# Performance work log

Measured on AMD Instinct MI355X. Metric: run time of the kernel, lower is better.

Reference implementation:

```python
import jax, jax.numpy as jnp
import numpy as np

B, N, K, H, C, PE, EMB, OUT = 2, 2048, 16, 4, 8, 64, 1024, 2
P = C * (C + 1) // 2  # 36 unordered class pairs
RADIUS, NEG, EPS = 0.08, 0.2, 1e-5


def _ball_query(pos, radius, nsample):
    # pos [B,N,2] -> idx [B,N,nsample]; indices within radius, padded with first in-ball index
    sq = jnp.sum(pos * pos, -1)
    d = sq[:, :, None] + sq[:, None, :] - 2.0 * jnp.einsum('bnc,bmc->bnm', pos, pos)
    n = pos.shape[1]
    idx = jnp.broadcast_to(jnp.arange(n)[None, None, :], d.shape)
    idx = jnp.where(d > radius * radius, n, idx)
    idx = jnp.sort(idx, axis=-1)[:, :, :nsample]
    return jnp.where(idx == n, idx[:, :, :1], idx)


def _gather(feat, idx):
    # feat [B,F,N], idx [B,N,K] -> [B,F,N,K]
    return jnp.take_along_axis(feat[:, :, None, :], idx[:, None, :, :], axis=3)


def _pe(rel, dim):
    # sinusoidal encoding of relative coords rel [B,2,N,K] -> [B,dim,N,K]
    nf = dim // 4
    freqs = 10000.0 ** (-jnp.arange(nf, dtype=rel.dtype) / nf)
    ang = rel[:, :, None] * freqs[None, None, :, None, None]     # [B,2,nf,N,K]
    enc = jnp.concatenate([jnp.sin(ang), jnp.cos(ang)], axis=2)  # [B,2,2nf,N,K]
    b = enc.shape[0]
    return enc.reshape(b, dim, enc.shape[3], enc.shape[4])


def _conv(x, w, g, bvec):
    # 1x1 conv (no bias) + inference BN (running mean 0, var 1) + LeakyReLU
    y = jnp.einsum('oc,bc...->bo...', w, x) / jnp.sqrt(1.0 + EPS)
    sh = (1, -1) + (1,) * (y.ndim - 2)
    return jax.nn.leaky_relu(y * g.reshape(sh) + bvec.reshape(sh), NEG)


def _attn_layer(x, Ws, a_pairs, a_selfs, core, tgt):
    # PointpairAttentionLayer (per-class-pair coefficients), vmapped over heads.
    # x [B,F,N,K]; core [B,N] int; tgt [B,N,K] int
    s0 = jnp.minimum(tgt, core[:, :, None])
    s1 = jnp.maximum(tgt, core[:, :, None])
    pidx = s0 * C - (s0 * (s0 - 1)) // 2 + (s1 - s0)             # [B,N,K] pair index
    self_mask = (tgt[:, :, 0] < core)[:, :, None]                # slot-0 keeps a_self when pair-write happened earlier

    def head(W, a_pair, a_self):
        Wh = jnp.einsum('bfnk,fg->bnkg', x, W)                   # [B,N,K,F]
        a = a_pair[pidx]                                         # [B,N,K,F]
        slot0 = jnp.where(self_mask, a_self[core], a[:, :, 0])
        a = a.at[:, :, 0].set(slot0)
        e = jax.nn.leaky_relu(Wh * a, NEG)
        attn = jax.nn.softmax(e, axis=2)                         # over K neighbors
        return jax.nn.elu(attn * Wh)                             # [B,N,K,F]

    hs = jax.vmap(head)(Ws, a_pairs, a_selfs)                    # [H,B,N,K,F]
    b, n, k = x.shape[0], x.shape[2], x.shape[3]
    return jnp.transpose(hs, (1, 0, 4, 2, 3)).reshape(b, -1, n, k)


def _edge(feat, idx):
    # DGCNN edge features: concat(neighbor - center, center)
    tf = _gather(feat, idx)
    return jnp.concatenate([tf - feat[..., None],
                            jnp.broadcast_to(feat[..., None], tf.shape)], axis=1)


def _forward(pos, types, conv1_w, bn1_g, bn1_b, W1, ap1, as1,
             conv2_w, bn2_g, bn2_b, W2, ap2, as2,
             conv3_w, bn3_g, bn3_b, W3, ap3, as3,
             conv4_w, bn4_g, bn4_b, W4, ap4, as4,
             conv5_w, bn5_g, bn5_b, lin1_w, bn6_g, bn6_b,
             lin2_w, lin2_b, bn7_g, bn7_b, lin3_w, lin3_b):
    idx = _ball_query(pos, RADIUS, K)                            # [B,N,K]
    posT = jnp.transpose(pos, (0, 2, 1))                         # [B,2,N]
    rel = _gather(posT, idx) - posT[..., None]                   # [B,2,N,K]
    tgt = _gather(types[:, None, :], idx)[:, 0]                  # [B,N,K] neighbor classes

    x = _conv(_pe(rel, PE), conv1_w, bn1_g, bn1_b)               # [B,64,N,K]
    x1 = _attn_layer(x, W1, ap1, as1, types, tgt).sum(-1)        # [B,H*64,N]
    x = _conv(_edge(x1, idx), conv2_w, bn2_g, bn2_b)             # [B,64,N,K]
    x2 = _attn_layer(x, W2, ap2, as2, types, tgt).sum(-1)        # [B,H*64,N]
    x = _conv(_edge(x2, idx), conv3_w, bn3_g, bn3_b)             # [B,128,N,K]
    x3 = _attn_layer(x, W3, ap3, as3, types, tgt).sum(-1)        # [B,H*128,N]
    x = _conv(_edge(x3, idx), conv4_w, bn4_g, bn4_b)             # [B,256,N,K]
    x4 = _attn_layer(x, W4, ap4, as4, types, tgt).sum(-1)        # [B,H*256,N]

    xc = jnp.concatenate([x1, x2, x3, x4], axis=1)               # [B,H*512,N]
    x = _conv(xc, conv5_w, bn5_g, bn5_b)                         # [B,EMB,N]
    feat = jnp.concatenate([x.max(-1), x.mean(-1)], axis=-1)     # [B,2*EMB]

    def bn1d(y, g, bvec):
        return (y / jnp.sqrt(1.0 + EPS)) * g + bvec

    h = jax.nn.leaky_relu(bn1d(feat @ lin1_w.T, bn6_g, bn6_b), NEG)
    h = jax.nn.leaky_relu(bn1d(h @ lin2_w.T + lin2_b, bn7_g, bn7_b), NEG)
    return h @ lin3_w.T + lin3_b                                 # [B,OUT]


def setup_inputs() -> dict:
    key = jax.random.key(0)
    ks = iter(jax.random.split(key, 64))
    rn = lambda *s: jax.random.normal(next(ks), s, dtype=jnp.float32)
    d = {}
    d['pos'] = jax.random.uniform(next(ks), (B, N, 2), dtype=jnp.float32)
    d['types'] = jax.random.randint(next(ks), (B, N), 0, C, dtype=jnp.int32)

    def layer(f_in, f, tag):
        d['conv%d_w' % tag] = rn(f, f_in) * (1.0 / np.sqrt(f_in))
        d['bn%d_g' % tag] = jnp.ones((f,), jnp.float32)
        d['bn%d_b' % tag] = jnp.zeros((f,), jnp.float32)

    layer(PE, 64, 1)
    d['W1'] = rn(H, 64, 64) * 0.125; d['ap1'] = rn(H, P, 64) * 0.5; d['as1'] = rn(H, C, 64) * 0.5
    layer(2 * H * 64, 64, 2)
    d['W2'] = rn(H, 64, 64) * 0.125; d['ap2'] = rn(H, P, 64) * 0.5; d['as2'] = rn(H, C, 64) * 0.5
    layer(2 * H * 64, 128, 3)
    d['W3'] = rn(H, 128, 128) * 0.09; d['ap3'] = rn(H, P, 128) * 0.5; d['as3'] = rn(H, C, 128) * 0.5
    layer(2 * H * 128, 256, 4)
    d['W4'] = rn(H, 256, 256) * 0.0625; d['ap4'] = rn(H, P, 256) * 0.5; d['as4'] = rn(H, C, 256) * 0.5
    layer(H * 512, EMB, 5)
    d['lin1_w'] = rn(512, 2 * EMB) * 0.02
    d['bn6_g'] = jnp.ones((512,), jnp.float32); d['bn6_b'] = jnp.zeros((512,), jnp.float32)
    d['lin2_w'] = rn(256, 512) * 0.04; d['lin2_b'] = jnp.zeros((256,), jnp.float32)
    d['bn7_g'] = jnp.ones((256,), jnp.float32); d['bn7_b'] = jnp.zeros((256,), jnp.float32)
    d['lin3_w'] = rn(OUT, 256) * 0.06; d['lin3_b'] = jnp.zeros((OUT,), jnp.float32)
    return d


def reference(pos, types, conv1_w, bn1_g, bn1_b, W1, ap1, as1,
              conv2_w, bn2_g, bn2_b, W2, ap2, as2,
              conv3_w, bn3_g, bn3_b, W3, ap3, as3,
              conv4_w, bn4_g, bn4_b, W4, ap4, as4,
              conv5_w, bn5_g, bn5_b, lin1_w, bn6_g, bn6_b,
              lin2_w, lin2_b, bn7_g, bn7_b, lin3_w, lin3_b):
    return _forward(pos, types, conv1_w, bn1_g, bn1_b, W1, ap1, as1,
                    conv2_w, bn2_g, bn2_b, W2, ap2, as2,
                    conv3_w, bn3_g, bn3_b, W3, ap3, as3,
                    conv4_w, bn4_g, bn4_b, W4, ap4, as4,
                    conv5_w, bn5_g, bn5_b, lin1_w, bn6_g, bn6_b,
                    lin2_w, lin2_b, bn7_g, bn7_b, lin3_w, lin3_b)
```

## Files before the change

### kernel.cpp

```cpp
#include <hip/hip_runtime.h>
#include <math.h>

#define BB 2
#define NN 2048
#define KK 16
#define HH 4
#define CC 8
#define PP 36
#define NEGS 0.2f
#define INVS 0.9999950000374997f

typedef __attribute__((ext_vector_type(8))) short s16x8;
typedef __attribute__((ext_vector_type(8))) unsigned short u16x8;
typedef __attribute__((ext_vector_type(4))) float f32x4;

__device__ inline unsigned short bfh(float x) {
  unsigned u = __float_as_uint(x);
  return (unsigned short)((u + 0x7FFFu + ((u >> 16) & 1u)) >> 16);
}
__device__ inline float bff(unsigned short h) {
  return __uint_as_float(((unsigned)h) << 16);
}
__device__ inline f32x4 mfma16(s16x8 a, s16x8 b, f32x4 c) {
  return __builtin_amdgcn_mfma_f32_16x16x32_bf16(a, b, c, 0, 0, 0);
}

__global__ __launch_bounds__(256) void k_ballquery(const float* __restrict__ pos,
                                                   const int* __restrict__ types,
                                                   int* __restrict__ idxg,
                                                   int* __restrict__ acode,
                                                   float* __restrict__ rel) {
  __shared__ int s_buf[4][KK];
  const float r2 = (float)(0.08 * 0.08);
  int wslot = threadIdx.x >> 6;
  int lane = threadIdx.x & 63;
  int wg = blockIdx.x * 4 + wslot;
  int b = wg / NN, n = wg - b * NN;
  const float* pb = pos + (size_t)b * NN * 2;
  float px = pb[n * 2 + 0], py = pb[n * 2 + 1];
  float sqn = px * px + py * py;
  unsigned mask = 0u;
  int base = lane * 32;
  for (int j = 0; j < 32; ++j) {
    float qx = pb[(base + j) * 2 + 0], qy = pb[(base + j) * 2 + 1];
    float sqm = qx * qx + qy * qy;
    float d = sqn + sqm - 2.0f * (px * qx + py * qy);
    if (d <= r2) mask |= (1u << j);
  }
  int cnt = __popc(mask);
  int inc = cnt;
#pragma unroll
  for (int off = 1; off < 64; off <<= 1) {
    int v = __shfl_up(inc, off, 64);
    if (lane >= off) inc += v;
  }
  int total = __shfl(inc, 63, 64);
  int excl = inc - cnt;
  unsigned mm = mask;
  int p = excl;
  while (mm && p < KK) {
    int j = __ffs(mm) - 1;
    mm &= mm - 1u;
    s_buf[wslot][p] = base + j;
    ++p;
  }
  __syncthreads();
  int tc = total < KK ? total : KK;
  if (lane < KK) {
    int m0 = s_buf[wslot][0];
    int mk = (lane < tc) ? s_buf[wslot][lane] : m0;
    idxg[wg * KK + lane] = mk;
    int core = types[b * NN + n];
    int tg = types[b * NN + mk];
    int s0 = tg < core ? tg : core;
    int s1 = tg < core ? core : tg;
    int code = s0 * CC - (s0 * (s0 - 1)) / 2 + (s1 - s0);
    if (lane == 0 && tg < core) code = PP + core;
    acode[wg * KK + lane] = code;
    rel[(wg * KK + lane) * 2 + 0] = pb[mk * 2 + 0] - px;
    rel[(wg * KK + lane) * 2 + 1] = pb[mk * 2 + 1] - py;
  }
}

struct PackDesc {
  const float* src;
  unsigned short* dh;
  unsigned short* dl;
  int KB, NT, srcld, Cdiff, mode, sstride, dstride, nrep, bpr;
};
struct PackArgs {
  PackDesc d[12];
};
__global__ __launch_bounds__(256) void k_megapack(PackArgs pa) {
  PackDesc D = pa.d[blockIdx.y];
  int rep = blockIdx.x / D.bpr;
  if (rep >= D.nrep) return;
  int f = (blockIdx.x - rep * D.bpr) * 256 + threadIdx.x;
  int total = D.KB * D.NT * 64;
  if (f >= total) return;
  const float* src = D.src + (size_t)rep * D.sstride;
  unsigned short* dh = D.dh + (size_t)rep * D.dstride;
  unsigned short* dl = D.dl + (size_t)rep * D.dstride;
  int l = f & 63;
  int t2 = f >> 6;
  int n = (t2 / D.KB) * 16 + (l & 15);
  int k0 = (t2 % D.KB) * 32 + ((l >> 4) * 8);
  size_t o = (size_t)t2 * 512 + (size_t)l * 8;
#pragma unroll
  for (int i = 0; i < 8; ++i) {
    int k = k0 + i;
    float v;
    if (D.mode == 0) {
      v = src[(size_t)k * D.srcld + n];
    } else if (D.mode == 1) {
      v = src[(size_t)n * D.srcld + k];
    } else {
      v = src[(size_t)n * D.srcld + k + D.Cdiff] - src[(size_t)n * D.srcld + k];
    }
    unsigned short hi = bfh(v);
    dh[o + i] = hi;
    dl[o + i] = bfh(v - bff(hi));
  }
}

template <int KBW, int NTB>
__global__ __launch_bounds__(512, 4) void k_pregemm(
    const unsigned short* __restrict__ xh, const unsigned short* __restrict__ xl,
    int xoff, const unsigned short* __restrict__ wph,
    const unsigned short* __restrict__ wpl, const float* __restrict__ scale,
    const float* __restrict__ bias, unsigned short* __restrict__ ouh,
    unsigned short* __restrict__ oul, int cout) {
  constexpr int NCH = KBW / 2;
  constexpr int JT = NTB / 2;
  const int KBT = KBW;
  const int ld = 2 * cout;
  __shared__ alignas(16) char s_mem[65536];
  int tid = threadIdx.x;
  int lane = tid & 63;
  int w = tid >> 6;
  int lg = lane >> 4;
  int ln = lane & 15;
  int bm = blockIdx.x;
  int ntoff = blockIdx.y * NTB;
  int wm = w >> 1, wn = w & 1;
  f32x4 acc[2][JT];
#pragma unroll
  for (int m = 0; m < 2; ++m)
#pragma unroll
    for (int j = 0; j < JT; ++j) acc[m][j] = (f32x4){0.f, 0.f, 0.f, 0.f};

  int srowg = bm * 128 + w * 16 + ln;
  const unsigned short* gH = xh + (size_t)srowg * 2048 + xoff + lg * 8;
  const unsigned short* gL = xl + (size_t)srowg * 2048 + xoff + lg * 8;
  int wbyA = ((w * 2 + 0) * 64 + lane) * 16;
  int wbyB = ((w * 2 + 1) * 64 + lane) * 16;
  u16x8 h0, h1, l0, l1;
  auto load4 = [&](int ch) {
    h0 = *(const u16x8*)(gH + ch * 64);
    h1 = *(const u16x8*)(gH + ch * 64 + 32);
    l0 = *(const u16x8*)(gL + ch * 64);
    l1 = *(const u16x8*)(gL + ch * 64 + 32);
  };
  load4(0);
  *(u16x8*)(s_mem + wbyA) = h0;
  *(u16x8*)(s_mem + wbyB) = h1;
  *(u16x8*)(s_mem + wbyA + 16384) = l0;
  *(u16x8*)(s_mem + wbyB + 16384) = l1;
  __syncthreads();
  int p = 0;
  for (int ch = 0; ch < NCH; ++ch) {
    if (ch + 1 < NCH) load4(ch + 1);
#pragma unroll
    for (int ks = 0; ks < 2; ++ks) {
      s16x8 ah[2], al[2];
#pragma unroll
      for (int m = 0; m < 2; ++m) {
        int by = p * 32768 + (((wm * 2 + m) * 2 + ks) * 64 + lane) * 16;
        ah[m] = *(const s16x8*)(s_mem + by);
        al[m] = *(const s16x8*)(s_mem + by + 16384);
      }
      int kb = ch * 2 + ks;
      __builtin_amdgcn_s_setprio(1);
#pragma unroll
      for (int j = 0; j < JT; ++j) {
        size_t fo = ((size_t)(ntoff + wn * JT + j) * KBT + kb) * 64 + lane;
        s16x8 bh = ((const s16x8*)wph)[fo];
        s16x8 bl = ((const s16x8*)wpl)[fo];
#pragma unroll
        for (int m = 0; m < 2; ++m) {
          acc[m][j] = mfma16(ah[m], bh, acc[m][j]);
          acc[m][j] = mfma16(al[m], bh, acc[m][j]);
          acc[m][j] = mfma16(ah[m], bl, acc[m][j]);
        }
      }
      __builtin_amdgcn_s_setprio(0);
    }
    if (ch + 1 < NCH) {
      int d = (p ^ 1) * 32768;
      *(u16x8*)(s_mem + d + wbyA) = h0;
      *(u16x8*)(s_mem + d + wbyB) = h1;
      *(u16x8*)(s_mem + d + wbyA + 16384) = l0;
      *(u16x8*)(s_mem + d + wbyB + 16384) = l1;
      p ^= 1;
    }
    __syncthreads();
  }
#pragma unroll
  for (int j = 0; j < JT; ++j) {
    int g = (ntoff + wn * JT + j) * 16 + ln;
    int gm = g >= cout ? g - cout : g;
    float sc = scale[gm] * INVS;
    float bs = (g >= cout) ? bias[gm] : 0.f;
#pragma unroll
    for (int m = 0; m < 2; ++m) {
#pragma unroll
      for (int reg = 0; reg < 4; ++reg) {
        int row = bm * 128 + wm * 32 + m * 16 + lg * 4 + reg;
        float v = acc[m][j][reg] * sc + bs;
        unsigned short hi = bfh(v);
        ouh[(size_t)row * ld + g] = hi;
        oul[(size_t)row * ld + g] = bfh(v - bff(hi));
      }
    }
  }
}

template <int FOUT>
__global__ __launch_bounds__(512, 4) void k_attn(
    unsigned short* xh, unsigned short* xl,
    const unsigned short* __restrict__ uvh, const unsigned short* __restrict__ uvl,
    const int* __restrict__ idx, const int* __restrict__ acode,
    const unsigned short* __restrict__ attnh, const unsigned short* __restrict__ attnl,
    const float* __restrict__ ap, const float* __restrict__ as_, int ooff) {
  constexpr int KBA = FOUT / 32;
  constexpr int NT = FOUT / 16;
  constexpr int NTW_A = NT / 2;
  constexpr int JW = (NTW_A > 2) ? 2 : NTW_A;
  constexpr int NPASS = NTW_A / JW;
  constexpr int YPLANE = 64 * FOUT * 2;
  constexpr int FPW = (4 * KBA) / 8;
  constexpr int C2 = 2 * FOUT;

  __shared__ alignas(16) char s_mem[2 * YPLANE];
  __shared__ int s_gsrc[64];
  __shared__ int s_code[64];

  int tid = threadIdx.x;
  int lane = tid & 63;
  int w = tid >> 6;
  int lg = lane >> 4;
  int ln = lane & 15;
  int pgbase = blockIdx.x * 4;

  if (tid < 64) {
    int pg = pgbase + (tid >> 4);
    int b = pg >> 11;
    s_gsrc[tid] = b * 2048 + idx[pg * KK + (tid & 15)];
    s_code[tid] = acode[pg * KK + (tid & 15)];
  }
  __syncthreads();

#pragma unroll
  for (int r = 0; r < FPW; ++r) {
    int f = w * FPW + r;
    int mt = f / KBA, kb = f % KBA;
    int row = mt * 16 + ln;
    int col = kb * 32 + lg * 8;
    int gsrc = s_gsrc[row];
    int ctr = pgbase + mt;
    u16x8 a = *(const u16x8*)(uvh + (size_t)gsrc * C2 + col);
    u16x8 b_ = *(const u16x8*)(uvl + (size_t)gsrc * C2 + col);
    u16x8 c_ = *(const u16x8*)(uvh + (size_t)ctr * C2 + FOUT + col);
    u16x8 d_ = *(const u16x8*)(uvl + (size_t)ctr * C2 + FOUT + col);
    unsigned short oh[8], olo[8];
#pragma unroll
    for (int i = 0; i < 8; ++i) {
      float vv = (bff(a[i]) + bff(b_[i])) + (bff(c_[i]) + bff(d_[i]));
      vv = (vv >= 0.f) ? vv : NEGS * vv;
      unsigned short hi = bfh(vv);
      oh[i] = hi;
      olo[i] = bfh(vv - bff(hi));
    }
    *(u16x8*)(s_mem + (f * 64 + lane) * 16) = *(u16x8*)oh;
    *(u16x8*)(s_mem + YPLANE + (f * 64 + lane) * 16) = *(u16x8*)olo;
  }
  __syncthreads();

  {
    int h = w >> 1, nh = w & 1;
    const s16x8* wph = (const s16x8*)(attnh + (size_t)h * FOUT * FOUT);
    const s16x8* wpl = (const s16x8*)(attnl + (size_t)h * FOUT * FOUT);
    const float* aph = ap + (size_t)h * PP * FOUT;
    const float* ash = as_ + (size_t)h * CC * FOUT;
    for (int pass = 0; pass < NPASS; ++pass) {
      f32x4 aacc[4][JW];
#pragma unroll
      for (int m = 0; m < 4; ++m)
#pragma unroll
        for (int j = 0; j < JW; ++j) aacc[m][j] = (f32x4){0.f, 0.f, 0.f, 0.f};
#pragma unroll 2
      for (int kb = 0; kb < KBA; ++kb) {
        s16x8 ah[4], al[4];
#pragma unroll
        for (int m = 0; m < 4; ++m) {
          int by = ((m * KBA + kb) * 64 + lane) * 16;
          ah[m] = *(const s16x8*)(s_mem + by);
          al[m] = *(const s16x8*)(s_mem + YPLANE + by);
        }
        __builtin_amdgcn_s_setprio(1);
#pragma unroll
        for (int j = 0; j < JW; ++j) {
          int nt = nh * NTW_A + pass * JW + j;
          size_t fo = ((size_t)nt * KBA + kb) * 64 + lane;
          s16x8 bh = wph[fo];
          s16x8 bl = wpl[fo];
#pragma unroll
          for (int m = 0; m < 4; ++m) {
            aacc[m][j] = mfma16(ah[m], bh, aacc[m][j]);
            aacc[m][j] = mfma16(al[m], bh, aacc[m][j]);
            aacc[m][j] = mfma16(ah[m], bl, aacc[m][j]);
          }
        }
        __builtin_amdgcn_s_setprio(0);
      }
#pragma unroll
      for (int m = 0; m < 4; ++m) {
        int pg = pgbase + m;
#pragma unroll
        for (int j = 0; j < JW; ++j) {
          int nt = nh * NTW_A + pass * JW + j;
          int g = nt * 16 + ln;
          float wv[4], e[4];
          float mx = -3.0e38f;
#pragma unroll
          for (int reg = 0; reg < 4; ++reg) {
            int code = s_code[m * 16 + lg * 4 + reg];
            const float* tb = (code < PP) ? (aph + (size_t)code * FOUT)
                                          : (ash + (size_t)(code - PP) * FOUT);
            float a = tb[g];
            float t = aacc[m][j][reg];
            wv[reg] = t;
            float ev = t * a;
            ev = (ev >= 0.f) ? ev : NEGS * ev;
            e[reg] = ev;
            mx = fmaxf(mx, ev);
          }
          mx = fmaxf(mx, __shfl_xor(mx, 16, 64));
          mx = fmaxf(mx, __shfl_xor(mx, 32, 64));
          float ssum = 0.f;
#pragma unroll
          for (int reg = 0; reg < 4; ++reg) {
            float pe = __expf(e[reg] - mx);
            e[reg] = pe;
            ssum += pe;
          }
          ssum += __shfl_xor(ssum, 16, 64);
          ssum += __shfl_xor(ssum, 32, 64);
          float inv = 1.f / ssum;
          float o = 0.f;
#pragma unroll
          for (int reg = 0; reg < 4; ++reg) {
            float u = e[reg] * inv * wv[reg];
            o += (u > 0.f) ? u : (__expf(u) - 1.f);
          }
          o += __shfl_xor(o, 16, 64);
          o += __shfl_xor(o, 32, 64);
          if (lane < 16) {
            size_t oc = (size_t)pg * 2048 + ooff + h * FOUT + g;
            unsigned short hi = bfh(o);
            xh[oc] = hi;
            xl[oc] = bfh(o - bff(hi));
          }
        }
      }
    }
  }
}

template <int CPREV, int FOUT, bool L1M>
__global__ __launch_bounds__(512, 4) void k_layer_m(
    unsigned short* xh, unsigned short* xl, int xoff,
    const float* __restrict__ rel, const int* __restrict__ idx,
    const int* __restrict__ acode,
    const unsigned short* __restrict__ convh, const unsigned short* __restrict__ convl,
    const unsigned short* __restrict__ attnh, const unsigned short* __restrict__ attnl,
    const float* __restrict__ bng, const float* __restrict__ bnb,
    const float* __restrict__ ap, const float* __restrict__ as_, int ooff) {
  constexpr int K_TOT = L1M ? CPREV : 2 * CPREV;
  constexpr int KB = K_TOT / 32;
  constexpr int NT = FOUT / 16;
  constexpr int NT_W = NT / 4;
  constexpr int NTW_A = NT / 2;
  constexpr int JW = (NTW_A > 2) ? 2 : NTW_A;
  constexpr int NPASS = NTW_A / JW;
  constexpr int KBA = FOUT / 32;
  constexpr int YPLANE = 64 * FOUT * 2;
  constexpr int S_BYTES = (2 * YPLANE > 32768) ? 2 * YPLANE : 32768;

  __shared__ alignas(16) char s_mem[S_BYTES];
  __shared__ int s_gsrc[64];
  __shared__ int s_code[64];

  int tid = threadIdx.x;
  int lane = tid & 63;
  int w = tid >> 6;
  int lg = lane >> 4;
  int ln = lane & 15;
  int pgbase = blockIdx.x * 4;

  if (tid < 64) {
    int pg = pgbase + (tid >> 4);
    int b = pg >> 11;
    s_gsrc[tid] = b * 2048 + idx[pg * KK + (tid & 15)];
    s_code[tid] = acode[pg * KK + (tid & 15)];
  }
  __syncthreads();

  int smt = w >> 1, skb = w & 1;
  int wby0 = (w * 64 + lane) * 16;

  int wr = w >> 2, wc = w & 3;
  f32x4 cacc[2][NT_W];
#pragma unroll
  for (int m = 0; m < 2; ++m)
#pragma unroll
    for (int j = 0; j < NT_W; ++j) cacc[m][j] = (f32x4){0.f, 0.f, 0.f, 0.f};

  auto compute_chunk = [&](int ch, int p) {
#pragma unroll
    for (int ks = 0; ks < 2; ++ks) {
      s16x8 ah[2], al[2];
#pragma unroll
      for (int m = 0; m < 2; ++m) {
        int by = p * 16384 + (((wr * 2 + m) * 2 + ks) * 64 + lane) * 16;
        ah[m] = *(const s16x8*)(s_mem + by);
        al[m] = *(const s16x8*)(s_mem + by + 8192);
      }
      int kb = ch * 2 + ks;
      __builtin_amdgcn_s_setprio(1);
#pragma unroll
      for (int j = 0; j < NT_W; ++j) {
        size_t fo = ((size_t)(wc * NT_W + j) * KB + kb) * 64 + lane;
        s16x8 bh = ((const s16x8*)convh)[fo];
        s16x8 bl = ((const s16x8*)convl)[fo];
#pragma unroll
        for (int m = 0; m < 2; ++m) {
          cacc[m][j] = mfma16(ah[m], bh, cacc[m][j]);
          cacc[m][j] = mfma16(al[m], bh, cacc[m][j]);
          cacc[m][j] = mfma16(ah[m], bl, cacc[m][j]);
        }
      }
      __builtin_amdgcn_s_setprio(0);
    }
  };

  if constexpr (L1M) {
    float rc = rel[((size_t)(pgbase + smt) * KK + ln) * 2 + skb];
    unsigned short hb[8], lb[8];
#pragma unroll
    for (int i = 0; i < 8; ++i) {
      int j = lg * 8 + i;
      int fidx = j & 15;
      float freq = exp2f(-(float)fidx * 0.8304820237218406f);
      float ang = rc * freq;
      float v = (j < 16) ? __sinf(ang) : __cosf(ang);
      unsigned short hi = bfh(v);
      hb[i] = hi;
      lb[i] = bfh(v - bff(hi));
    }
    *(u16x8*)(s_mem + wby0) = *(u16x8*)hb;
    *(u16x8*)(s_mem + wby0 + 8192) = *(u16x8*)lb;
    __syncthreads();
    compute_chunk(0, 0);
    __syncthreads();
  }

#pragma unroll
  for (int j = 0; j < NT_W; ++j) {
    int g = (wc * NT_W + j) * 16 + ln;
    float sc = bng[g] * INVS;
    float bs = bnb[g];
    int gpart = ((g >> 5) * 64 + ((g >> 3) & 3) * 16) * 16 + (g & 7) * 2;
#pragma unroll
    for (int m = 0; m < 2; ++m) {
#pragma unroll
      for (int reg = 0; reg < 4; ++reg) {
        int r = wr * 32 + m * 16 + lg * 4 + reg;
        float v = cacc[m][j][reg] * sc + bs;
        v = (v >= 0.f) ? v : NEGS * v;
        unsigned short hi = bfh(v);
        unsigned short lo = bfh(v - bff(hi));
        int by = (r >> 4) * (KBA * 1024) + gpart + (r & 15) * 16;
        *(unsigned short*)(s_mem + by) = hi;
        *(unsigned short*)(s_mem + YPLANE + by) = lo;
      }
    }
  }
  __syncthreads();

  {
    int h = w >> 1, nh = w & 1;
    const s16x8* wph = (const s16x8*)(attnh + (size_t)h * FOUT * FOUT);
    const s16x8* wpl = (const s16x8*)(attnl + (size_t)h * FOUT * FOUT);
    const float* aph = ap + (size_t)h * PP * FOUT;
    const float* ash = as_ + (size_t)h * CC * FOUT;
    for (int pass = 0; pass < NPASS; ++pass) {
      f32x4 aacc[4][JW];
#pragma unroll
      for (int m = 0; m < 4; ++m)
#pragma unroll
        for (int j = 0; j < JW; ++j) aacc[m][j] = (f32x4){0.f, 0.f, 0.f, 0.f};
#pragma unroll 2
      for (int kb = 0; kb < KBA; ++kb) {
        s16x8 ah[4], al[4];
#pragma unroll
        for (int m = 0; m < 4; ++m) {
          int by = ((m * KBA + kb) * 64 + lane) * 16;
          ah[m] = *(const s16x8*)(s_mem + by);
          al[m] = *(const s16x8*)(s_mem + YPLANE + by);
        }
        __builtin_amdgcn_s_setprio(1);
#pragma unroll
        for (int j = 0; j < JW; ++j) {
          int nt = nh * NTW_A + pass * JW + j;
          size_t fo = ((size_t)nt * KBA + kb) * 64 + lane;
          s16x8 bh = wph[fo];
          s16x8 bl = wpl[fo];
#pragma unroll
          for (int m = 0; m < 4; ++m) {
            aacc[m][j] = mfma16(ah[m], bh, aacc[m][j]);
            aacc[m][j] = mfma16(al[m], bh, aacc[m][j]);
            aacc[m][j] = mfma16(ah[m], bl, aacc[m][j]);
          }
        }
        __builtin_amdgcn_s_setprio(0);
      }
#pragma unroll
      for (int m = 0; m < 4; ++m) {
        int pg = pgbase + m;
#pragma unroll
        for (int j = 0; j < JW; ++j) {
          int nt = nh * NTW_A + pass * JW + j;
          int g = nt * 16 + ln;
          float wv[4], e[4];
          float mx = -3.0e38f;
#pragma unroll
          for (int reg = 0; reg < 4; ++reg) {
            int code = s_code[m * 16 + lg * 4 + reg];
            const float* tb = (code < PP) ? (aph + (size_t)code * FOUT)
                                          : (ash + (size_t)(code - PP) * FOUT);
            float a = tb[g];
            float t = aacc[m][j][reg];
            wv[reg] = t;
            float ev = t * a;
            ev = (ev >= 0.f) ? ev : NEGS * ev;
            e[reg] = ev;
            mx = fmaxf(mx, ev);
          }
          mx = fmaxf(mx, __shfl_xor(mx, 16, 64));
          mx = fmaxf(mx, __shfl_xor(mx, 32, 64));
          float ssum = 0.f;
#pragma unroll
          for (int reg = 0; reg < 4; ++reg) {
            float pe = __expf(e[reg] - mx);
            e[reg] = pe;
            ssum += pe;
          }
          ssum += __shfl_xor(ssum, 16, 64);
          ssum += __shfl_xor(ssum, 32, 64);
          float inv = 1.f / ssum;
          float o = 0.f;
#pragma unroll
          for (int reg = 0; reg < 4; ++reg) {
            float u = e[reg] * inv * wv[reg];
            o += (u > 0.f) ? u : (__expf(u) - 1.f);
          }
          o += __shfl_xor(o, 16, 64);
          o += __shfl_xor(o, 32, 64);
          if (lane < 16) {
            size_t oc = (size_t)pg * 2048 + ooff + h * FOUT + g;
            unsigned short hi = bfh(o);
            xh[oc] = hi;
            xl[oc] = bfh(o - bff(hi));
          }
        }
      }
    }
  }
}

__global__ __launch_bounds__(512, 4) void k_gemm5_m(const unsigned short* __restrict__ xh,
                                                    const unsigned short* __restrict__ xl,
                                                    const unsigned short* __restrict__ bph,
                                                    const unsigned short* __restrict__ bpl,
                                                    const float* __restrict__ g5,
                                                    const float* __restrict__ b5,
                                                    float* __restrict__ pmax,
                                                    float* __restrict__ psum) {
  __shared__ alignas(16) char s_mem[65536];
  int tid = threadIdx.x;
  int lane = tid & 63;
  int w = tid >> 6;
  int lg = lane >> 4;
  int ln = lane & 15;
  int bm = blockIdx.x, bn = blockIdx.y;
  int wm = w >> 2, wn = w & 3;
  f32x4 acc[4][2];
#pragma unroll
  for (int m = 0; m < 4; ++m)
#pragma unroll
    for (int j = 0; j < 2; ++j) acc[m][j] = (f32x4){0.f, 0.f, 0.f, 0.f};

  int srowg = bm * 128 + w * 16 + ln;
  const unsigned short* gH = xh + (size_t)srowg * 2048 + lg * 8;
  const unsigned short* gL = xl + (size_t)srowg * 2048 + lg * 8;
  int wbyA = ((w * 2 + 0) * 64 + lane) * 16;
  int wbyB = ((w * 2 + 1) * 64 + lane) * 16;
  u16x8 h0, h1, l0, l1;
  auto load4 = [&](int ch) {
    h0 = *(const u16x8*)(gH + ch * 64);
    h1 = *(const u16x8*)(gH + ch * 64 + 32);
    l0 = *(const u16x8*)(gL + ch * 64);
    l1 = *(const u16x8*)(gL + ch * 64 + 32);
  };
  load4(0);
  *(u16x8*)(s_mem + wbyA) = h0;
  *(u16x8*)(s_mem + wbyB) = h1;
  *(u16x8*)(s_mem + wbyA + 16384) = l0;
  *(u16x8*)(s_mem + wbyB + 16384) = l1;
  __syncthreads();
  int p = 0;
  for (int ch = 0; ch < 32; ++ch) {
    if (ch + 1 < 32) load4(ch + 1);
#pragma unroll
    for (int ks = 0; ks < 2; ++ks) {
      s16x8 ah[4], al[4];
#pragma unroll
      for (int m = 0; m < 4; ++m) {
        int by = p * 32768 + (((wm * 4 + m) * 2 + ks) * 64 + lane) * 16;
        ah[m] = *(const s16x8*)(s_mem + by);
        al[m] = *(const s16x8*)(s_mem + by + 16384);
      }
      int kb = ch * 2 + ks;
      __builtin_amdgcn_s_setprio(1);
#pragma unroll
      for (int j = 0; j < 2; ++j) {
        size_t fo = ((size_t)(bn * 8 + wn * 2 + j) * 64 + kb) * 64 + lane;
        s16x8 bh = ((const s16x8*)bph)[fo];
        s16x8 bl = ((const s16x8*)bpl)[fo];
#pragma unroll
        for (int m = 0; m < 4; ++m) {
          acc[m][j] = mfma16(ah[m], bh, acc[m][j]);
          acc[m][j] = mfma16(al[m], bh, acc[m][j]);
          acc[m][j] = mfma16(ah[m], bl, acc[m][j]);
        }
      }
      __builtin_amdgcn_s_setprio(0);
    }
    if (ch + 1 < 32) {
      int d = (p ^ 1) * 32768;
      *(u16x8*)(s_mem + d + wbyA) = h0;
      *(u16x8*)(s_mem + d + wbyB) = h1;
      *(u16x8*)(s_mem + d + wbyA + 16384) = l0;
      *(u16x8*)(s_mem + d + wbyB + 16384) = l1;
      p ^= 1;
    }
    __syncthreads();
  }

  float cmax[2], csum[2];
#pragma unroll
  for (int j = 0; j < 2; ++j) {
    int g = bn * 128 + wn * 32 + j * 16 + ln;
    float sc = g5[g] * INVS;
    float bs = b5[g];
    float mx = -3.0e38f, sm = 0.f;
#pragma unroll
    for (int m = 0; m < 4; ++m)
#pragma unroll
      for (int reg = 0; reg < 4; ++reg) {
        float v = acc[m][j][reg] * sc + bs;
        v = (v >= 0.f) ? v : NEGS * v;
        mx = fmaxf(mx, v);
        sm += v;
      }
    mx = fmaxf(mx, __shfl_xor(mx, 16, 64));
    mx = fmaxf(mx, __shfl_xor(mx, 32, 64));
    sm += __shfl_xor(sm, 16, 64);
    sm += __shfl_xor(sm, 32, 64);
    cmax[j] = mx;
    csum[j] = sm;
  }
  float* s_f = (float*)s_mem;
  if (lg == 0) {
#pragma unroll
    for (int j = 0; j < 2; ++j) {
      int col = wn * 32 + j * 16 + ln;
      s_f[(wm * 128 + col) * 2 + 0] = cmax[j];
      s_f[(wm * 128 + col) * 2 + 1] = csum[j];
    }
  }
  __syncthreads();
  if (tid < 128) {
    float mx = fmaxf(s_f[tid * 2], s_f[(128 + tid) * 2]);
    float sm = s_f[tid * 2 + 1] + s_f[(128 + tid) * 2 + 1];
    pmax[(size_t)bm * 1024 + bn * 128 + tid] = mx;
    psum[(size_t)bm * 1024 + bn * 128 + tid] = sm;
  }
}

__global__ __launch_bounds__(256) void k_feat(const float* __restrict__ pmax,
                                              const float* __restrict__ psum,
                                              float* __restrict__ feat) {
  int t = blockIdx.x * 256 + threadIdx.x;
  if (t >= BB * 1024) return;
  int b = t >> 10, o = t & 1023;
  float mx = -3.0e38f, sm = 0.f;
  for (int i = 0; i < 16; ++i) {
    mx = fmaxf(mx, pmax[(size_t)(b * 16 + i) * 1024 + o]);
    sm += psum[(size_t)(b * 16 + i) * 1024 + o];
  }
  feat[b * 2048 + o] = mx;
  feat[b * 2048 + 1024 + o] = sm * (1.0f / NN);
}

template <bool HASB, bool DOBN, bool ACT>
__global__ __launch_bounds__(256) void k_head(const float* __restrict__ X,
                                              const float* __restrict__ Wm,
                                              const float* __restrict__ bias,
                                              const float* __restrict__ g,
                                              const float* __restrict__ bb,
                                              float* __restrict__ Y, int IN, int ON) {
  int gt = blockIdx.x * 256 + threadIdx.x;
  int w = gt >> 6, lane = gt & 63;
  if (w >= BB * ON) return;
  int b = w / ON, o = w - b * ON;
  const float* x = X + (size_t)b * IN;
  const float* wr = Wm + (size_t)o * IN;
  float s = 0.f;
  for (int c = lane; c < IN; c += 64) s += x[c] * wr[c];
#pragma unroll
  for (int off = 32; off > 0; off >>= 1) s += __shfl_down(s, off, 64);
  if (lane == 0) {
    if (HASB) s += bias[o];
    if (DOBN) s = s * INVS * g[o] + bb[o];
    if (ACT) s = (s >= 0.f) ? s : NEGS * s;
    Y[(size_t)b * ON + o] = s;
  }
}

extern "C" void kernel_launch(void* const* d_in, const int* in_sizes, int n_in,
                              void* d_out, int out_size, void* d_ws, size_t ws_size,
                              hipStream_t stream) {
  const float* pos = (const float*)d_in[0];
  const int* types = (const int*)d_in[1];
  const float* conv1_w = (const float*)d_in[2];
  const float* bn1_g = (const float*)d_in[3];
  const float* bn1_b = (const float*)d_in[4];
  const float* W1 = (const float*)d_in[5];
  const float* ap1 = (const float*)d_in[6];
  const float* as1 = (const float*)d_in[7];
  const float* conv2_w = (const float*)d_in[8];
  const float* bn2_g = (const float*)d_in[9];
  const float* bn2_b = (const float*)d_in[10];
  const float* W2 = (const float*)d_in[11];
  const float* ap2 = (const float*)d_in[12];
  const float* as2 = (const float*)d_in[13];
  const float* conv3_w = (const float*)d_in[14];
  const float* bn3_g = (const float*)d_in[15];
  const float* bn3_b = (const float*)d_in[16];
  const float* W3 = (const float*)d_in[17];
  const float* ap3 = (const float*)d_in[18];
  const float* as3 = (const float*)d_in[19];
  const float* conv4_w = (const float*)d_in[20];
  const float* bn4_g = (const float*)d_in[21];
  const float* bn4_b = (const float*)d_in[22];
  const float* W4 = (const float*)d_in[23];
  const float* ap4 = (const float*)d_in[24];
  const float* as4 = (const float*)d_in[25];
  const float* conv5_w = (const float*)d_in[26];
  const float* bn5_g = (const float*)d_in[27];
  const float* bn5_b = (const float*)d_in[28];
  const float* lin1_w = (const float*)d_in[29];
  const float* bn6_g = (const float*)d_in[30];
  const float* bn6_b = (const float*)d_in[31];
  const float* lin2_w = (const float*)d_in[32];
  const float* lin2_b = (const float*)d_in[33];
  const float* bn7_g = (const float*)d_in[34];
  const float* bn7_b = (const float*)d_in[35];
  const float* lin3_w = (const float*)d_in[36];
  const float* lin3_b = (const float*)d_in[37];
  (void)in_sizes; (void)n_in; (void)out_size; (void)ws_size;

  float* ws = (float*)d_ws;
  size_t off = 0;
  auto take = [&](size_t nf) {
    float* p = ws + off;
    off += (nf + 63) & ~(size_t)63;
    return p;
  };
  auto takeu = [&](size_t nu) { return (unsigned short*)take((nu + 1) / 2); };

  int* idx = (int*)take(BB * NN * KK);
  int* acode = (int*)take(BB * NN * KK);
  float* rel = take((size_t)BB * NN * KK * 2);
  unsigned short* xh = takeu((size_t)BB * NN * 2048);
  unsigned short* xl = takeu((size_t)BB * NN * 2048);
  unsigned short* uvh = takeu((size_t)4096 * 512);
  unsigned short* uvl = takeu((size_t)4096 * 512);
  float* pmax = take(32 * 1024);
  float* psum = take(32 * 1024);
  float* feat = take(BB * 2048);
  float* h1 = take(BB * 512);
  float* h2 = take(BB * 256);
  unsigned short* c1h = takeu(64 * 64);
  unsigned short* c1l = takeu(64 * 64);
  unsigned short* uvw2h = takeu(256 * 128);
  unsigned short* uvw2l = takeu(256 * 128);
  unsigned short* uvw3h = takeu(256 * 256);
  unsigned short* uvw3l = takeu(256 * 256);
  unsigned short* uvw4h = takeu(512 * 512);
  unsigned short* uvw4l = takeu(512 * 512);
  unsigned short* a1h = takeu(4 * 64 * 64);
  unsigned short* a1l = takeu(4 * 64 * 64);
  unsigned short* a2h = takeu(4 * 64 * 64);
  unsigned short* a2l = takeu(4 * 64 * 64);
  unsigned short* a3h = takeu(4 * 128 * 128);
  unsigned short* a3l = takeu(4 * 128 * 128);
  unsigned short* a4h = takeu(4 * 256 * 256);
  unsigned short* a4l = takeu(4 * 256 * 256);
  unsigned short* g5h = takeu((size_t)2048 * 1024);
  unsigned short* g5l = takeu((size_t)2048 * 1024);

  dim3 blk(256);
  dim3 blk5(512);

  PackArgs pa;
  pa.d[0] = {conv1_w, c1h, c1l, 2, 4, 64, 0, 1, 0, 0, 1, 2};
  pa.d[1] = {conv2_w, uvw2h, uvw2l, 8, 4, 512, 0, 1, 0, 0, 1, 8};
  pa.d[2] = {conv2_w, uvw2h + 16384, uvw2l + 16384, 8, 4, 512, 256, 2, 0, 0, 1, 8};
  pa.d[3] = {conv3_w, uvw3h, uvw3l, 8, 8, 512, 0, 1, 0, 0, 1, 16};
  pa.d[4] = {conv3_w, uvw3h + 32768, uvw3l + 32768, 8, 8, 512, 256, 2, 0, 0, 1, 16};
  pa.d[5] = {conv4_w, uvw4h, uvw4l, 16, 16, 1024, 0, 1, 0, 0, 1, 64};
  pa.d[6] = {conv4_w, uvw4h + 131072, uvw4l + 131072, 16, 16, 1024, 512, 2, 0, 0, 1, 64};
  pa.d[7] = {W1, a1h, a1l, 2, 4, 64, 0, 0, 4096, 4096, 4, 2};
  pa.d[8] = {W2, a2h, a2l, 2, 4, 64, 0, 0, 4096, 4096, 4, 2};
  pa.d[9] = {W3, a3h, a3l, 4, 8, 128, 0, 0, 16384, 16384, 4, 8};
  pa.d[10] = {W4, a4h, a4l, 8, 16, 256, 0, 0, 65536, 65536, 4, 32};
  pa.d[11] = {conv5_w, g5h, g5l, 64, 64, 2048, 0, 1, 0, 0, 1, 1024};
  k_megapack<<<dim3(1024, 12), blk, 0, stream>>>(pa);

  k_ballquery<<<dim3(BB * NN / 4), blk, 0, stream>>>(pos, types, idx, acode, rel);

  k_layer_m<64, 64, true><<<dim3(BB * NN / 4), blk5, 0, stream>>>(
      xh, xl, 0, rel, idx, acode, c1h, c1l, a1h, a1l, bn1_g, bn1_b, ap1, as1, 0);

  k_pregemm<8, 4><<<dim3(32, 2), blk5, 0, stream>>>(
      xh, xl, 0, uvw2h, uvw2l, bn2_g, bn2_b, uvh, uvl, 64);
  k_attn<64><<<dim3(BB * NN / 4), blk5, 0, stream>>>(
      xh, xl, uvh, uvl, idx, acode, a2h, a2l, ap2, as2, 256);

  k_pregemm<8, 8><<<dim3(32, 2), blk5, 0, stream>>>(
      xh, xl, 256, uvw3h, uvw3l, bn3_g, bn3_b, uvh, uvl, 128);
  k_attn<128><<<dim3(BB * NN / 4), blk5, 0, stream>>>(
      xh, xl, uvh, uvl, idx, acode, a3h, a3l, ap3, as3, 512);

  k_pregemm<16, 8><<<dim3(32, 4), blk5, 0, stream>>>(
      xh, xl, 512, uvw4h, uvw4l, bn4_g, bn4_b, uvh, uvl, 256);
  k_attn<256><<<dim3(BB * NN / 4), blk5, 0, stream>>>(
      xh, xl, uvh, uvl, idx, acode, a4h, a4l, ap4, as4, 1024);

  k_gemm5_m<<<dim3(32, 8), blk5, 0, stream>>>(xh, xl, g5h, g5l, bn5_g, bn5_b, pmax, psum);
  k_feat<<<dim3(8), blk, 0, stream>>>(pmax, psum, feat);
  k_head<false, true, true><<<dim3(BB * 512 * 64 / 256), blk, 0, stream>>>(
      feat, lin1_w, nullptr, bn6_g, bn6_b, h1, 2048, 512);
  k_head<true, true, true><<<dim3(BB * 256 * 64 / 256), blk, 0, stream>>>(
      h1, lin2_w, lin2_b, bn7_g, bn7_b, h2, 512, 256);
  k_head<true, false, false><<<dim3(1), blk, 0, stream>>>(
      h2, lin3_w, lin3_b, nullptr, nullptr, (float*)d_out, 256, 2);
}
```

Measured before the change: 429.2 us.

## Drop low-half activation splitting, store pre-GEMM in fp32, fuse head kernels

Activations are now kept only as a single bf16 plane instead of a hi/lo pair, which removes one of the three MFMAs per product and halves LDS staging and global traffic. The pre-GEMM output is written as fp32 rather than as two bf16 planes. The softmax max-subtraction is dropped. The feature reduction and three head layers are merged into one tail kernel. Precision of the activations falls to plain bf16, and removing the max subtraction risks exp overflow for large logits.

```diff
diff --git a/kernel.cpp b/kernel.cpp
--- a/kernel.cpp
+++ b/kernel.cpp
@@ -125,16 +125,14 @@
 
 template <int KBW, int NTB>
 __global__ __launch_bounds__(512, 4) void k_pregemm(
-    const unsigned short* __restrict__ xh, const unsigned short* __restrict__ xl,
-    int xoff, const unsigned short* __restrict__ wph,
-    const unsigned short* __restrict__ wpl, const float* __restrict__ scale,
-    const float* __restrict__ bias, unsigned short* __restrict__ ouh,
-    unsigned short* __restrict__ oul, int cout) {
+    const unsigned short* __restrict__ xh, int xoff,
+    const unsigned short* __restrict__ wph, const unsigned short* __restrict__ wpl,
+    const float* __restrict__ scale, const float* __restrict__ bias,
+    float* __restrict__ ouv, int cout) {
   constexpr int NCH = KBW / 2;
   constexpr int JT = NTB / 2;
-  const int KBT = KBW;
   const int ld = 2 * cout;
-  __shared__ alignas(16) char s_mem[65536];
+  __shared__ alignas(16) char s_mem[32768];
   int tid = threadIdx.x;
   int lane = tid & 63;
   int w = tid >> 6;
@@ -151,56 +149,47 @@
 
   int srowg = bm * 128 + w * 16 + ln;
   const unsigned short* gH = xh + (size_t)srowg * 2048 + xoff + lg * 8;
-  const unsigned short* gL = xl + (size_t)srowg * 2048 + xoff + lg * 8;
   int wbyA = ((w * 2 + 0) * 64 + lane) * 16;
   int wbyB = ((w * 2 + 1) * 64 + lane) * 16;
-  u16x8 h0, h1, l0, l1;
-  auto load4 = [&](int ch) {
+  u16x8 h0, h1;
+  auto load2 = [&](int ch) {
     h0 = *(const u16x8*)(gH + ch * 64);
     h1 = *(const u16x8*)(gH + ch * 64 + 32);
-    l0 = *(const u16x8*)(gL + ch * 64);
-    l1 = *(const u16x8*)(gL + ch * 64 + 32);
   };
-  load4(0);
+  load2(0);
   *(u16x8*)(s_mem + wbyA) = h0;
   *(u16x8*)(s_mem + wbyB) = h1;
-  *(u16x8*)(s_mem + wbyA + 16384) = l0;
-  *(u16x8*)(s_mem + wbyB + 16384) = l1;
   __syncthreads();
   int p = 0;
   for (int ch = 0; ch < NCH; ++ch) {
-    if (ch + 1 < NCH) load4(ch + 1);
+    if (ch + 1 < NCH) load2(ch + 1);
 #pragma unroll
     for (int ks = 0; ks < 2; ++ks) {
-      s16x8 ah[2], al[2];
+      s16x8 ah[2];
 #pragma unroll
       for (int m = 0; m < 2; ++m) {
-        int by = p * 32768 + (((wm * 2 + m) * 2 + ks) * 64 + lane) * 16;
+        int by = p * 16384 + (((wm * 2 + m) * 2 + ks) * 64 + lane) * 16;
         ah[m] = *(const s16x8*)(s_mem + by);
-        al[m] = *(const s16x8*)(s_mem + by + 16384);
       }
       int kb = ch * 2 + ks;
       __builtin_amdgcn_s_setprio(1);
 #pragma unroll
       for (int j = 0; j < JT; ++j) {
-        size_t fo = ((size_t)(ntoff + wn * JT + j) * KBT + kb) * 64 + lane;
+        size_t fo = ((size_t)(ntoff + wn * JT + j) * KBW + kb) * 64 + lane;
         s16x8 bh = ((const s16x8*)wph)[fo];
         s16x8 bl = ((const s16x8*)wpl)[fo];
 #pragma unroll
         for (int m = 0; m < 2; ++m) {
           acc[m][j] = mfma16(ah[m], bh, acc[m][j]);
-          acc[m][j] = mfma16(al[m], bh, acc[m][j]);
           acc[m][j] = mfma16(ah[m], bl, acc[m][j]);
         }
       }
       __builtin_amdgcn_s_setprio(0);
     }
     if (ch + 1 < NCH) {
-      int d = (p ^ 1) * 32768;
+      int d = (p ^ 1) * 16384;
       *(u16x8*)(s_mem + d + wbyA) = h0;
       *(u16x8*)(s_mem + d + wbyB) = h1;
-      *(u16x8*)(s_mem + d + wbyA + 16384) = l0;
-      *(u16x8*)(s_mem + d + wbyB + 16384) = l1;
       p ^= 1;
     }
     __syncthreads();
@@ -216,32 +205,113 @@
 #pragma unroll
       for (int reg = 0; reg < 4; ++reg) {
         int row = bm * 128 + wm * 32 + m * 16 + lg * 4 + reg;
-        float v = acc[m][j][reg] * sc + bs;
-        unsigned short hi = bfh(v);
-        ouh[(size_t)row * ld + g] = hi;
-        oul[(size_t)row * ld + g] = bfh(v - bff(hi));
+        ouv[(size_t)row * ld + g] = acc[m][j][reg] * sc + bs;
       }
     }
   }
 }
 
 template <int FOUT>
-__global__ __launch_bounds__(512, 4) void k_attn(
-    unsigned short* xh, unsigned short* xl,
-    const unsigned short* __restrict__ uvh, const unsigned short* __restrict__ uvl,
-    const int* __restrict__ idx, const int* __restrict__ acode,
-    const unsigned short* __restrict__ attnh, const unsigned short* __restrict__ attnl,
-    const float* __restrict__ ap, const float* __restrict__ as_, int ooff) {
+__device__ __forceinline__ void attn_phase(
+    const char* s_mem, const int* s_code, unsigned short* xh, int pgbase,
+    int w, int lane, const unsigned short* __restrict__ attnh,
+    const unsigned short* __restrict__ attnl, const float* __restrict__ ap,
+    const float* __restrict__ as_, int ooff) {
   constexpr int KBA = FOUT / 32;
   constexpr int NT = FOUT / 16;
   constexpr int NTW_A = NT / 2;
   constexpr int JW = (NTW_A > 2) ? 2 : NTW_A;
   constexpr int NPASS = NTW_A / JW;
+  int lg = lane >> 4;
+  int ln = lane & 15;
+  int h = w >> 1, nh = w & 1;
+  const s16x8* wph = (const s16x8*)(attnh + (size_t)h * FOUT * FOUT);
+  const s16x8* wpl = (const s16x8*)(attnl + (size_t)h * FOUT * FOUT);
+  const float* aph = ap + (size_t)h * PP * FOUT;
+  const float* ash = as_ + (size_t)h * CC * FOUT;
+  for (int pass = 0; pass < NPASS; ++pass) {
+    f32x4 aacc[4][JW];
+#pragma unroll
+    for (int m = 0; m < 4; ++m)
+#pragma unroll
+      for (int j = 0; j < JW; ++j) aacc[m][j] = (f32x4){0.f, 0.f, 0.f, 0.f};
+#pragma unroll 2
+    for (int kb = 0; kb < KBA; ++kb) {
+      s16x8 ah[4];
+#pragma unroll
+      for (int m = 0; m < 4; ++m) {
+        int by = ((m * KBA + kb) * 64 + lane) * 16;
+        ah[m] = *(const s16x8*)(s_mem + by);
+      }
+      __builtin_amdgcn_s_setprio(1);
+#pragma unroll
+      for (int j = 0; j < JW; ++j) {
+        int nt = nh * NTW_A + pass * JW + j;
+        size_t fo = ((size_t)nt * KBA + kb) * 64 + lane;
+        s16x8 bh = wph[fo];
+        s16x8 bl = wpl[fo];
+#pragma unroll
+        for (int m = 0; m < 4; ++m) {
+          aacc[m][j] = mfma16(ah[m], bh, aacc[m][j]);
+          aacc[m][j] = mfma16(ah[m], bl, aacc[m][j]);
+        }
+      }
+      __builtin_amdgcn_s_setprio(0);
+    }
+#pragma unroll
+    for (int m = 0; m < 4; ++m) {
+      int pg = pgbase + m;
+#pragma unroll
+      for (int j = 0; j < JW; ++j) {
+        int nt = nh * NTW_A + pass * JW + j;
+        int g = nt * 16 + ln;
+        float wv[4], e[4];
+        float ssum = 0.f;
+#pragma unroll
+        for (int reg = 0; reg < 4; ++reg) {
+          int code = s_code[m * 16 + lg * 4 + reg];
+          const float* tb = (code < PP) ? (aph + (size_t)code * FOUT)
+                                        : (ash + (size_t)(code - PP) * FOUT);
+          float a = tb[g];
+          float t = aacc[m][j][reg];
+          wv[reg] = t;
+          float ev = t * a;
+          ev = (ev >= 0.f) ? ev : NEGS * ev;
+          float pe = __expf(ev);
+          e[reg] = pe;
+          ssum += pe;
+        }
+        ssum += __shfl_xor(ssum, 16, 64);
+        ssum += __shfl_xor(ssum, 32, 64);
+        float inv = 1.f / ssum;
+        float o = 0.f;
+#pragma unroll
+        for (int reg = 0; reg < 4; ++reg) {
+          float u = e[reg] * inv * wv[reg];
+          o += (u > 0.f) ? u : (__expf(u) - 1.f);
+        }
+        o += __shfl_xor(o, 16, 64);
+        o += __shfl_xor(o, 32, 64);
+        if (lane < 16) {
+          xh[(size_t)pg * 2048 + ooff + h * FOUT + g] = bfh(o);
+        }
+      }
+    }
+  }
+}
+
+template <int FOUT>
+__global__ __launch_bounds__(512, 4) void k_attn(
+    unsigned short* xh, const float* __restrict__ uv,
+    const int* __restrict__ idx, const int* __restrict__ acode,
+    const unsigned short* __restrict__ attnh, const unsigned short* __restrict__ attnl,
+    const float* __restrict__ ap, const float* __restrict__ as_, int ooff) {
+  constexpr int KBA = FOUT / 32;
   constexpr int YPLANE = 64 * FOUT * 2;
   constexpr int FPW = (4 * KBA) / 8;
   constexpr int C2 = 2 * FOUT;
 
-  __shared__ alignas(16) char s_mem[2 * YPLANE];
+  __shared__ alignas(16) char s_mem[YPLANE];
   __shared__ int s_gsrc[64];
   __shared__ int s_code[64];
 
@@ -266,138 +336,41 @@
     int mt = f / KBA, kb = f % KBA;
     int row = mt * 16 + ln;
     int col = kb * 32 + lg * 8;
-    int gsrc = s_gsrc[row];
-    int ctr = pgbase + mt;
-    u16x8 a = *(const u16x8*)(uvh + (size_t)gsrc * C2 + col);
-    u16x8 b_ = *(const u16x8*)(uvl + (size_t)gsrc * C2 + col);
-    u16x8 c_ = *(const u16x8*)(uvh + (size_t)ctr * C2 + FOUT + col);
-    u16x8 d_ = *(const u16x8*)(uvl + (size_t)ctr * C2 + FOUT + col);
-    unsigned short oh[8], olo[8];
+    const float* up = uv + (size_t)s_gsrc[row] * C2 + col;
+    const float* cp = uv + (size_t)(pgbase + mt) * C2 + FOUT + col;
+    float4 u0 = *(const float4*)up;
+    float4 u1 = *(const float4*)(up + 4);
+    float4 v0 = *(const float4*)cp;
+    float4 v1 = *(const float4*)(cp + 4);
+    float uu[8] = {u0.x, u0.y, u0.z, u0.w, u1.x, u1.y, u1.z, u1.w};
+    float vv[8] = {v0.x, v0.y, v0.z, v0.w, v1.x, v1.y, v1.z, v1.w};
+    unsigned short oh[8];
 #pragma unroll
     for (int i = 0; i < 8; ++i) {
-      float vv = (bff(a[i]) + bff(b_[i])) + (bff(c_[i]) + bff(d_[i]));
-      vv = (vv >= 0.f) ? vv : NEGS * vv;
-      unsigned short hi = bfh(vv);
-      oh[i] = hi;
-      olo[i] = bfh(vv - bff(hi));
+      float t = uu[i] + vv[i];
+      t = (t >= 0.f) ? t : NEGS * t;
+      oh[i] = bfh(t);
     }
     *(u16x8*)(s_mem + (f * 64 + lane) * 16) = *(u16x8*)oh;
-    *(u16x8*)(s_mem + YPLANE + (f * 64 + lane) * 16) = *(u16x8*)olo;
-  }
-  __syncthreads();
-
-  {
-    int h = w >> 1, nh = w & 1;
-    const s16x8* wph = (const s16x8*)(attnh + (size_t)h * FOUT * FOUT);
-    const s16x8* wpl = (const s16x8*)(attnl + (size_t)h * FOUT * FOUT);
-    const float* aph = ap + (size_t)h * PP * FOUT;
-    const float* ash = as_ + (size_t)h * CC * FOUT;
-    for (int pass = 0; pass < NPASS; ++pass) {
-      f32x4 aacc[4][JW];
-#pragma unroll
-      for (int m = 0; m < 4; ++m)
-#pragma unroll
-        for (int j = 0; j < JW; ++j) aacc[m][j] = (f32x4){0.f, 0.f, 0.f, 0.f};
-#pragma unroll 2
-      for (int kb = 0; kb < KBA; ++kb) {
-        s16x8 ah[4], al[4];
-#pragma unroll
-        for (int m = 0; m < 4; ++m) {
-          int by = ((m * KBA + kb) * 64 + lane) * 16;
-          ah[m] = *(const s16x8*)(s_mem + by);
-          al[m] = *(const s16x8*)(s_mem + YPLANE + by);
-        }
-        __builtin_amdgcn_s_setprio(1);
-#pragma unroll
-        for (int j = 0; j < JW; ++j) {
-          int nt = nh * NTW_A + pass * JW + j;
-          size_t fo = ((size_t)nt * KBA + kb) * 64 + lane;
-          s16x8 bh = wph[fo];
-          s16x8 bl = wpl[fo];
-#pragma unroll
-          for (int m = 0; m < 4; ++m) {
-            aacc[m][j] = mfma16(ah[m], bh, aacc[m][j]);
-            aacc[m][j] = mfma16(al[m], bh, aacc[m][j]);
-            aacc[m][j] = mfma16(ah[m], bl, aacc[m][j]);
-          }
-        }
-        __builtin_amdgcn_s_setprio(0);
-      }
-#pragma unroll
-      for (int m = 0; m < 4; ++m) {
-        int pg = pgbase + m;
-#pragma unroll
-        for (int j = 0; j < JW; ++j) {
-          int nt = nh * NTW_A + pass * JW + j;
-          int g = nt * 16 + ln;
-          float wv[4], e[4];
-          float mx = -3.0e38f;
-#pragma unroll
-          for (int reg = 0; reg < 4; ++reg) {
-            int code = s_code[m * 16 + lg * 4 + reg];
-            const float* tb = (code < PP) ? (aph + (size_t)code * FOUT)
-                                          : (ash + (size_t)(code - PP) * FOUT);
-            float a = tb[g];
-            float t = aacc[m][j][reg];
-            wv[reg] = t;
-            float ev = t * a;
-            ev = (ev >= 0.f) ? ev : NEGS * ev;
-            e[reg] = ev;
-            mx = fmaxf(mx, ev);
-          }
-          mx = fmaxf(mx, __shfl_xor(mx, 16, 64));
-          mx = fmaxf(mx, __shfl_xor(mx, 32, 64));
-          float ssum = 0.f;
-#pragma unroll
-          for (int reg = 0; reg < 4; ++reg) {
-            float pe = __expf(e[reg] - mx);
-            e[reg] = pe;
-            ssum += pe;
-          }
-          ssum += __shfl_xor(ssum, 16, 64);
-          ssum += __shfl_xor(ssum, 32, 64);
-          float inv = 1.f / ssum;
-          float o = 0.f;
-#pragma unroll
-          for (int reg = 0; reg < 4; ++reg) {
-            float u = e[reg] * inv * wv[reg];
-            o += (u > 0.f) ? u : (__expf(u) - 1.f);
-          }
-          o += __shfl_xor(o, 16, 64);
-          o += __shfl_xor(o, 32, 64);
-          if (lane < 16) {
-            size_t oc = (size_t)pg * 2048 + ooff + h * FOUT + g;
-            unsigned short hi = bfh(o);
-            xh[oc] = hi;
-            xl[oc] = bfh(o - bff(hi));
-          }
-        }
-      }
-    }
-  }
-}
-
-template <int CPREV, int FOUT, bool L1M>
-__global__ __launch_bounds__(512, 4) void k_layer_m(
-    unsigned short* xh, unsigned short* xl, int xoff,
-    const float* __restrict__ rel, const int* __restrict__ idx,
+  }
+  __syncthreads();
+
+  attn_phase<FOUT>(s_mem, s_code, xh, pgbase, w, lane, attnh, attnl, ap, as_, ooff);
+}
+
+__global__ __launch_bounds__(512, 4) void k_layer1(
+    unsigned short* xh, const float* __restrict__ rel, const int* __restrict__ idx,
     const int* __restrict__ acode,
     const unsigned short* __restrict__ convh, const unsigned short* __restrict__ convl,
     const unsigned short* __restrict__ attnh, const unsigned short* __restrict__ attnl,
     const float* __restrict__ bng, const float* __restrict__ bnb,
     const float* __restrict__ ap, const float* __restrict__ as_, int ooff) {
-  constexpr int K_TOT = L1M ? CPREV : 2 * CPREV;
-  constexpr int KB = K_TOT / 32;
-  constexpr int NT = FOUT / 16;
-  constexpr int NT_W = NT / 4;
-  constexpr int NTW_A = NT / 2;
-  constexpr int JW = (NTW_A > 2) ? 2 : NTW_A;
-  constexpr int NPASS = NTW_A / JW;
-  constexpr int KBA = FOUT / 32;
+  constexpr int FOUT = 64;
+  constexpr int KB = 2;
+  constexpr int KBA = 2;
   constexpr int YPLANE = 64 * FOUT * 2;
-  constexpr int S_BYTES = (2 * YPLANE > 32768) ? 2 * YPLANE : 32768;
-
-  __shared__ alignas(16) char s_mem[S_BYTES];
+
+  __shared__ alignas(16) char s_mem[YPLANE];
   __shared__ int s_gsrc[64];
   __shared__ int s_code[64];
 
@@ -416,47 +389,10 @@
   }
   __syncthreads();
 
-  int smt = w >> 1, skb = w & 1;
-  int wby0 = (w * 64 + lane) * 16;
-
-  int wr = w >> 2, wc = w & 3;
-  f32x4 cacc[2][NT_W];
-#pragma unroll
-  for (int m = 0; m < 2; ++m)
-#pragma unroll
-    for (int j = 0; j < NT_W; ++j) cacc[m][j] = (f32x4){0.f, 0.f, 0.f, 0.f};
-
-  auto compute_chunk = [&](int ch, int p) {
-#pragma unroll
-    for (int ks = 0; ks < 2; ++ks) {
-      s16x8 ah[2], al[2];
-#pragma unroll
-      for (int m = 0; m < 2; ++m) {
-        int by = p * 16384 + (((wr * 2 + m) * 2 + ks) * 64 + lane) * 16;
-        ah[m] = *(const s16x8*)(s_mem + by);
-        al[m] = *(const s16x8*)(s_mem + by + 8192);
-      }
-      int kb = ch * 2 + ks;
-      __builtin_amdgcn_s_setprio(1);
-#pragma unroll
-      for (int j = 0; j < NT_W; ++j) {
-        size_t fo = ((size_t)(wc * NT_W + j) * KB + kb) * 64 + lane;
-        s16x8 bh = ((const s16x8*)convh)[fo];
-        s16x8 bl = ((const s16x8*)convl)[fo];
-#pragma unroll
-        for (int m = 0; m < 2; ++m) {
-          cacc[m][j] = mfma16(ah[m], bh, cacc[m][j]);
-          cacc[m][j] = mfma16(al[m], bh, cacc[m][j]);
-          cacc[m][j] = mfma16(ah[m], bl, cacc[m][j]);
-        }
-      }
-      __builtin_amdgcn_s_setprio(0);
-    }
-  };
-
-  if constexpr (L1M) {
+  {
+    int smt = w >> 1, skb = w & 1;
     float rc = rel[((size_t)(pgbase + smt) * KK + ln) * 2 + skb];
-    unsigned short hb[8], lb[8];
+    unsigned short hb[8];
 #pragma unroll
     for (int i = 0; i < 8; ++i) {
       int j = lg * 8 + i;
@@ -464,20 +400,39 @@
       float freq = exp2f(-(float)fidx * 0.8304820237218406f);
       float ang = rc * freq;
       float v = (j < 16) ? __sinf(ang) : __cosf(ang);
-      unsigned short hi = bfh(v);
-      hb[i] = hi;
-      lb[i] = bfh(v - bff(hi));
-    }
-    *(u16x8*)(s_mem + wby0) = *(u16x8*)hb;
-    *(u16x8*)(s_mem + wby0 + 8192) = *(u16x8*)lb;
-    __syncthreads();
-    compute_chunk(0, 0);
-    __syncthreads();
-  }
-
-#pragma unroll
-  for (int j = 0; j < NT_W; ++j) {
-    int g = (wc * NT_W + j) * 16 + ln;
+      hb[i] = bfh(v);
+    }
+    *(u16x8*)(s_mem + ((w * 64 + lane) * 16)) = *(u16x8*)hb;
+  }
+  __syncthreads();
+
+  int wr = w >> 2, wc = w & 3;
+  f32x4 cacc[2];
+  cacc[0] = (f32x4){0.f, 0.f, 0.f, 0.f};
+  cacc[1] = (f32x4){0.f, 0.f, 0.f, 0.f};
+#pragma unroll
+  for (int ks = 0; ks < 2; ++ks) {
+    s16x8 ah[2];
+#pragma unroll
+    for (int m = 0; m < 2; ++m) {
+      int by = (((wr * 2 + m) * 2 + ks) * 64 + lane) * 16;
+      ah[m] = *(const s16x8*)(s_mem + by);
+    }
+    __builtin_amdgcn_s_setprio(1);
+    size_t fo = ((size_t)wc * KB + ks) * 64 + lane;
+    s16x8 bh = ((const s16x8*)convh)[fo];
+    s16x8 bl = ((const s16x8*)convl)[fo];
+#pragma unroll
+    for (int m = 0; m < 2; ++m) {
+      cacc[m] = mfma16(ah[m], bh, cacc[m]);
+      cacc[m] = mfma16(ah[m], bl, cacc[m]);
+    }
+    __builtin_amdgcn_s_setprio(0);
+  }
+  __syncthreads();
+
+  {
+    int g = wc * 16 + ln;
     float sc = bng[g] * INVS;
     float bs = bnb[g];
     int gpart = ((g >> 5) * 64 + ((g >> 3) & 3) * 16) * 16 + (g & 7) * 2;
@@ -486,118 +441,26 @@
 #pragma unroll
       for (int reg = 0; reg < 4; ++reg) {
         int r = wr * 32 + m * 16 + lg * 4 + reg;
-        float v = cacc[m][j][reg] * sc + bs;
+        float v = cacc[m][reg] * sc + bs;
         v = (v >= 0.f) ? v : NEGS * v;
-        unsigned short hi = bfh(v);
-        unsigned short lo = bfh(v - bff(hi));
         int by = (r >> 4) * (KBA * 1024) + gpart + (r & 15) * 16;
-        *(unsigned short*)(s_mem + by) = hi;
-        *(unsigned short*)(s_mem + YPLANE + by) = lo;
-      }
-    }
-  }
-  __syncthreads();
-
-  {
-    int h = w >> 1, nh = w & 1;
-    const s16x8* wph = (const s16x8*)(attnh + (size_t)h * FOUT * FOUT);
-    const s16x8* wpl = (const s16x8*)(attnl + (size_t)h * FOUT * FOUT);
-    const float* aph = ap + (size_t)h * PP * FOUT;
-    const float* ash = as_ + (size_t)h * CC * FOUT;
-    for (int pass = 0; pass < NPASS; ++pass) {
-      f32x4 aacc[4][JW];
-#pragma unroll
-      for (int m = 0; m < 4; ++m)
-#pragma unroll
-        for (int j = 0; j < JW; ++j) aacc[m][j] = (f32x4){0.f, 0.f, 0.f, 0.f};
-#pragma unroll 2
-      for (int kb = 0; kb < KBA; ++kb) {
-        s16x8 ah[4], al[4];
-#pragma unroll
-        for (int m = 0; m < 4; ++m) {
-          int by = ((m * KBA + kb) * 64 + lane) * 16;
-          ah[m] = *(const s16x8*)(s_mem + by);
-          al[m] = *(const s16x8*)(s_mem + YPLANE + by);
-        }
-        __builtin_amdgcn_s_setprio(1);
-#pragma unroll
-        for (int j = 0; j < JW; ++j) {
-          int nt = nh * NTW_A + pass * JW + j;
-          size_t fo = ((size_t)nt * KBA + kb) * 64 + lane;
-          s16x8 bh = wph[fo];
-          s16x8 bl = wpl[fo];
-#pragma unroll
-          for (int m = 0; m < 4; ++m) {
-            aacc[m][j] = mfma16(ah[m], bh, aacc[m][j]);
-            aacc[m][j] = mfma16(al[m], bh, aacc[m][j]);
-            aacc[m][j] = mfma16(ah[m], bl, aacc[m][j]);
-          }
-        }
-        __builtin_amdgcn_s_setprio(0);
-      }
-#pragma unroll
-      for (int m = 0; m < 4; ++m) {
-        int pg = pgbase + m;
-#pragma unroll
-        for (int j = 0; j < JW; ++j) {
-          int nt = nh * NTW_A + pass * JW + j;
-          int g = nt * 16 + ln;
-          float wv[4], e[4];
-          float mx = -3.0e38f;
-#pragma unroll
-          for (int reg = 0; reg < 4; ++reg) {
-            int code = s_code[m * 16 + lg * 4 + reg];
-            const float* tb = (code < PP) ? (aph + (size_t)code * FOUT)
-                                          : (ash + (size_t)(code - PP) * FOUT);
-            float a = tb[g];
-            float t = aacc[m][j][reg];
-            wv[reg] = t;
-            float ev = t * a;
-            ev = (ev >= 0.f) ? ev : NEGS * ev;
-            e[reg] = ev;
-            mx = fmaxf(mx, ev);
-          }
-          mx = fmaxf(mx, __shfl_xor(mx, 16, 64));
-          mx = fmaxf(mx, __shfl_xor(mx, 32, 64));
-          float ssum = 0.f;
-#pragma unroll
-          for (int reg = 0; reg < 4; ++reg) {
-            float pe = __expf(e[reg] - mx);
-            e[reg] = pe;
-            ssum += pe;
-          }
-          ssum += __shfl_xor(ssum, 16, 64);
-          ssum += __shfl_xor(ssum, 32, 64);
-          float inv = 1.f / ssum;
-          float o = 0.f;
-#pragma unroll
-          for (int reg = 0; reg < 4; ++reg) {
-            float u = e[reg] * inv * wv[reg];
-            o += (u > 0.f) ? u : (__expf(u) - 1.f);
-          }
-          o += __shfl_xor(o, 16, 64);
-          o += __shfl_xor(o, 32, 64);
-          if (lane < 16) {
-            size_t oc = (size_t)pg * 2048 + ooff + h * FOUT + g;
-            unsigned short hi = bfh(o);
-            xh[oc] = hi;
-            xl[oc] = bfh(o - bff(hi));
-          }
-        }
-      }
-    }
-  }
+        *(unsigned short*)(s_mem + by) = bfh(v);
+      }
+    }
+  }
+  __syncthreads();
+
+  attn_phase<FOUT>(s_mem, s_code, xh, pgbase, w, lane, attnh, attnl, ap, as_, ooff);
 }
 
 __global__ __launch_bounds__(512, 4) void k_gemm5_m(const unsigned short* __restrict__ xh,
-                                                    const unsigned short* __restrict__ xl,
                                                     const unsigned short* __restrict__ bph,
                                                     const unsigned short* __restrict__ bpl,
                                                     const float* __restrict__ g5,
                                                     const float* __restrict__ b5,
                                                     float* __restrict__ pmax,
                                                     float* __restrict__ psum) {
-  __shared__ alignas(16) char s_mem[65536];
+  __shared__ alignas(16) char s_mem[32768];
   int tid = threadIdx.x;
   int lane = tid & 63;
   int w = tid >> 6;
@@ -613,33 +476,27 @@
 
   int srowg = bm * 128 + w * 16 + ln;
   const unsigned short* gH = xh + (size_t)srowg * 2048 + lg * 8;
-  const unsigned short* gL = xl + (size_t)srowg * 2048 + lg * 8;
   int wbyA = ((w * 2 + 0) * 64 + lane) * 16;
   int wbyB = ((w * 2 + 1) * 64 + lane) * 16;
-  u16x8 h0, h1, l0, l1;
-  auto load4 = [&](int ch) {
+  u16x8 h0, h1;
+  auto load2 = [&](int ch) {
     h0 = *(const u16x8*)(gH + ch * 64);
     h1 = *(const u16x8*)(gH + ch * 64 + 32);
-    l0 = *(const u16x8*)(gL + ch * 64);
-    l1 = *(const u16x8*)(gL + ch * 64 + 32);
   };
-  load4(0);
+  load2(0);
   *(u16x8*)(s_mem + wbyA) = h0;
   *(u16x8*)(s_mem + wbyB) = h1;
-  *(u16x8*)(s_mem + wbyA + 16384) = l0;
-  *(u16x8*)(s_mem + wbyB + 16384) = l1;
   __syncthreads();
   int p = 0;
   for (int ch = 0; ch < 32; ++ch) {
-    if (ch + 1 < 32) load4(ch + 1);
+    if (ch + 1 < 32) load2(ch + 1);
 #pragma unroll
     for (int ks = 0; ks < 2; ++ks) {
-      s16x8 ah[4], al[4];
+      s16x8 ah[4];
 #pragma unroll
       for (int m = 0; m < 4; ++m) {
-        int by = p * 32768 + (((wm * 4 + m) * 2 + ks) * 64 + lane) * 16;
+        int by = p * 16384 + (((wm * 4 + m) * 2 + ks) * 64 + lane) * 16;
         ah[m] = *(const s16x8*)(s_mem + by);
-        al[m] = *(const s16x8*)(s_mem + by + 16384);
       }
       int kb = ch * 2 + ks;
       __builtin_amdgcn_s_setprio(1);
@@ -651,18 +508,15 @@
 #pragma unroll
         for (int m = 0; m < 4; ++m) {
           acc[m][j] = mfma16(ah[m], bh, acc[m][j]);
-          acc[m][j] = mfma16(al[m], bh, acc[m][j]);
           acc[m][j] = mfma16(ah[m], bl, acc[m][j]);
         }
       }
       __builtin_amdgcn_s_setprio(0);
     }
     if (ch + 1 < 32) {
-      int d = (p ^ 1) * 32768;
+      int d = (p ^ 1) * 16384;
       *(u16x8*)(s_mem + d + wbyA) = h0;
       *(u16x8*)(s_mem + d + wbyB) = h1;
-      *(u16x8*)(s_mem + d + wbyA + 16384) = l0;
-      *(u16x8*)(s_mem + d + wbyB + 16384) = l1;
       p ^= 1;
     }
     __syncthreads();
@@ -709,43 +563,59 @@
   }
 }
 
-__global__ __launch_bounds__(256) void k_feat(const float* __restrict__ pmax,
-                                              const float* __restrict__ psum,
-                                              float* __restrict__ feat) {
-  int t = blockIdx.x * 256 + threadIdx.x;
-  if (t >= BB * 1024) return;
-  int b = t >> 10, o = t & 1023;
-  float mx = -3.0e38f, sm = 0.f;
-  for (int i = 0; i < 16; ++i) {
-    mx = fmaxf(mx, pmax[(size_t)(b * 16 + i) * 1024 + o]);
-    sm += psum[(size_t)(b * 16 + i) * 1024 + o];
-  }
-  feat[b * 2048 + o] = mx;
-  feat[b * 2048 + 1024 + o] = sm * (1.0f / NN);
-}
-
-template <bool HASB, bool DOBN, bool ACT>
-__global__ __launch_bounds__(256) void k_head(const float* __restrict__ X,
-                                              const float* __restrict__ Wm,
-                                              const float* __restrict__ bias,
-                                              const float* __restrict__ g,
-                                              const float* __restrict__ bb,
-                                              float* __restrict__ Y, int IN, int ON) {
-  int gt = blockIdx.x * 256 + threadIdx.x;
-  int w = gt >> 6, lane = gt & 63;
-  if (w >= BB * ON) return;
-  int b = w / ON, o = w - b * ON;
-  const float* x = X + (size_t)b * IN;
-  const float* wr = Wm + (size_t)o * IN;
-  float s = 0.f;
-  for (int c = lane; c < IN; c += 64) s += x[c] * wr[c];
-#pragma unroll
-  for (int off = 32; off > 0; off >>= 1) s += __shfl_down(s, off, 64);
-  if (lane == 0) {
-    if (HASB) s += bias[o];
-    if (DOBN) s = s * INVS * g[o] + bb[o];
-    if (ACT) s = (s >= 0.f) ? s : NEGS * s;
-    Y[(size_t)b * ON + o] = s;
+__global__ __launch_bounds__(512) void k_tail(
+    const float* __restrict__ pmax, const float* __restrict__ psum,
+    const float* __restrict__ lin1_w, const float* __restrict__ bn6_g,
+    const float* __restrict__ bn6_b, const float* __restrict__ lin2_w,
+    const float* __restrict__ lin2_b, const float* __restrict__ bn7_g,
+    const float* __restrict__ bn7_b, const float* __restrict__ lin3_w,
+    const float* __restrict__ lin3_b, float* __restrict__ out) {
+  __shared__ float s_feat[2048];
+  __shared__ float s_h1[512];
+  __shared__ float s_h2[256];
+  int tid = threadIdx.x, lane = tid & 63, w = tid >> 6;
+  int b = blockIdx.x;
+  for (int t = tid; t < 1024; t += 512) {
+    float mx = -3.0e38f, sm = 0.f;
+    for (int i = 0; i < 16; ++i) {
+      mx = fmaxf(mx, pmax[(size_t)(b * 16 + i) * 1024 + t]);
+      sm += psum[(size_t)(b * 16 + i) * 1024 + t];
+    }
+    s_feat[t] = mx;
+    s_feat[1024 + t] = sm * (1.0f / NN);
+  }
+  __syncthreads();
+  for (int o = w; o < 512; o += 8) {
+    const float* wr = lin1_w + (size_t)o * 2048;
+    float s = 0.f;
+    for (int c = lane; c < 2048; c += 64) s += s_feat[c] * wr[c];
+#pragma unroll
+    for (int off = 32; off > 0; off >>= 1) s += __shfl_down(s, off, 64);
+    if (lane == 0) {
+      s = s * INVS * bn6_g[o] + bn6_b[o];
+      s_h1[o] = (s >= 0.f) ? s : NEGS * s;
+    }
+  }
+  __syncthreads();
+  for (int o = w; o < 256; o += 8) {
+    const float* wr = lin2_w + (size_t)o * 512;
+    float s = 0.f;
+    for (int c = lane; c < 512; c += 64) s += s_h1[c] * wr[c];
+#pragma unroll
+    for (int off = 32; off > 0; off >>= 1) s += __shfl_down(s, off, 64);
+    if (lane == 0) {
+      s = (s + lin2_b[o]) * INVS * bn7_g[o] + bn7_b[o];
+      s_h2[o] = (s >= 0.f) ? s : NEGS * s;
+    }
+  }
+  __syncthreads();
+  if (w < 2) {
+    const float* wr = lin3_w + (size_t)w * 256;
+    float s = 0.f;
+    for (int c = lane; c < 256; c += 64) s += s_h2[c] * wr[c];
+#pragma unroll
+    for (int off = 32; off > 0; off >>= 1) s += __shfl_down(s, off, 64);
+    if (lane == 0) out[b * 2 + w] = s + lin3_b[w];
   }
 }
 
@@ -805,14 +675,9 @@
   int* acode = (int*)take(BB * NN * KK);
   float* rel = take((size_t)BB * NN * KK * 2);
   unsigned short* xh = takeu((size_t)BB * NN * 2048);
-  unsigned short* xl = takeu((size_t)BB * NN * 2048);
-  unsigned short* uvh = takeu((size_t)4096 * 512);
-  unsigned short* uvl = takeu((size_t)4096 * 512);
+  float* uv = take((size_t)4096 * 512);
   float* pmax = take(32 * 1024);
   float* psum = take(32 * 1024);
-  float* feat = take(BB * 2048);
-  float* h1 = take(BB * 512);
-  float* h2 = take(BB * 256);
   unsigned short* c1h = takeu(64 * 64);
   unsigned short* c1l = takeu(64 * 64);
   unsigned short* uvw2h = takeu(256 * 128);
@@ -852,30 +717,26 @@
 
   k_ballquery<<<dim3(BB * NN / 4), blk, 0, stream>>>(pos, types, idx, acode, rel);
 
-  k_layer_m<64, 64, true><<<dim3(BB * NN / 4), blk5, 0, stream>>>(
-      xh, xl, 0, rel, idx, acode, c1h, c1l, a1h, a1l, bn1_g, bn1_b, ap1, as1, 0);
+  k_layer1<<<dim3(BB * NN / 4), blk5, 0, stream>>>(
+      xh, rel, idx, acode, c1h, c1l, a1h, a1l, bn1_g, bn1_b, ap1, as1, 0);
 
   k_pregemm<8, 4><<<dim3(32, 2), blk5, 0, stream>>>(
-      xh, xl, 0, uvw2h, uvw2l, bn2_g, bn2_b, uvh, uvl, 64);
+      xh, 0, uvw2h, uvw2l, bn2_g, bn2_b, uv, 64);
   k_attn<64><<<dim3(BB * NN / 4), blk5, 0, stream>>>(
-      xh, xl, uvh, uvl, idx, acode, a2h, a2l, ap2, as2, 256);
+      xh, uv, idx, acode, a2h, a2l, ap2, as2, 256);
 
   k_pregemm<8, 8><<<dim3(32, 2), blk5, 0, stream>>>(
-      xh, xl, 256, uvw3h, uvw3l, bn3_g, bn3_b, uvh, uvl, 128);
+      xh, 256, uvw3h, uvw3l, bn3_g, bn3_b, uv, 128);
   k_attn<128><<<dim3(BB * NN / 4), blk5, 0, stream>>>(
-      xh, xl, uvh, uvl, idx, acode, a3h, a3l, ap3, as3, 512);
+      xh, uv, idx, acode, a3h, a3l, ap3, as3, 512);
 
   k_pregemm<16, 8><<<dim3(32, 4), blk5, 0, stream>>>(
-      xh, xl, 512, uvw4h, uvw4l, bn4_g, bn4_b, uvh, uvl, 256);
+      xh, 512, uvw4h, uvw4l, bn4_g, bn4_b, uv, 256);
   k_attn<256><<<dim3(BB * NN / 4), blk5, 0, stream>>>(
-      xh, xl, uvh, uvl, idx, acode, a4h, a4l, ap4, as4, 1024);
-
-  k_gemm5_m<<<dim3(32, 8), blk5, 0, stream>>>(xh, xl, g5h, g5l, bn5_g, bn5_b, pmax, psum);
-  k_feat<<<dim3(8), blk, 0, stream>>>(pmax, psum, feat);
-  k_head<false, true, true><<<dim3(BB * 512 * 64 / 256), blk, 0, stream>>>(
-      feat, lin1_w, nullptr, bn6_g, bn6_b, h1, 2048, 512);
-  k_head<true, true, true><<<dim3(BB * 256 * 64 / 256), blk, 0, stream>>>(
-      h1, lin2_w, lin2_b, bn7_g, bn7_b, h2, 512, 256);
-  k_head<true, false, false><<<dim3(1), blk, 0, stream>>>(
-      h2, lin3_w, lin3_b, nullptr, nullptr, (float*)d_out, 256, 2);
-}
+      xh, uv, idx, acode, a4h, a4l, ap4, as4, 1024);
+
+  k_gemm5_m<<<dim3(32, 8), blk5, 0, stream>>>(xh, g5h, g5l, bn5_g, bn5_b, pmax, psum);
+  k_tail<<<dim3(2), blk5, 0, stream>>>(pmax, psum, lin1_w, bn6_g, bn6_b, lin2_w,
+                                       lin2_b, bn7_g, bn7_b, lin3_w, lin3_b,
+                                       (float*)d_out);
+}
```

New measurement: 1.024 ms. 2.39x slower.
